# Kernel optimization log

Hardware: AMD Instinct MI355X
Metric: run time of the kernel (lower is better)

## Reference

```python
import jax, jax.numpy as jnp
import numpy as np

EMB = 512
H1, H2 = 300, 100


def setup_inputs() -> dict:
    key = jax.random.key(0)
    ks = jax.random.split(key, 12)
    B, N, M = 2, 256, 256
    inp = {
        "action_embedding": jax.random.normal(ks[0], (B, EMB, N), jnp.float32),
        "anchor_embedding": jax.random.normal(ks[1], (B, EMB, M), jnp.float32),
        "action_points": jax.random.normal(ks[2], (B, 3, N), jnp.float32),
        "anchor_points": jax.random.normal(ks[3], (B, 3, M), jnp.float32),
        # MLPKernel params: Linear(1024,300), Linear(300,100), Linear(100,1), stored as [in,out]
        "W1": jax.random.normal(ks[4], (2 * EMB, H1), jnp.float32) / np.sqrt(2 * EMB),
        "b1": jax.random.normal(ks[5], (H1,), jnp.float32) * 0.01,
        "W2": jax.random.normal(ks[6], (H1, H2), jnp.float32) / np.sqrt(H1),
        "b2": jax.random.normal(ks[7], (H2,), jnp.float32) * 0.01,
        "W3": jax.random.normal(ks[8], (H2, 1), jnp.float32) / np.sqrt(H2),
        "b3": jax.random.normal(ks[9], (1,), jnp.float32) * 0.01,
    }
    return inp


def _pairwise_radii(Phi_A, Phi_B, W1, b1, W2, b2, W3, b3):
    # MLPKernel: softplus((mlp(cat(a,b)) + mlp(cat(b,a))) / 2) over all (n, m) pairs.
    # Split first linear: cat(x1,x2) @ W1 == x1 @ Wa + x2 @ Wb  (no [B,N,M,1024] materialization).
    F = Phi_A.shape[-1]
    Wa, Wb = W1[:F], W1[F:]
    hA_a = jnp.einsum('bnf,fh->bnh', Phi_A, Wa)
    hA_b = jnp.einsum('bnf,fh->bnh', Phi_A, Wb)
    hB_a = jnp.einsum('bmf,fh->bmh', Phi_B, Wa)
    hB_b = jnp.einsum('bmf,fh->bmh', Phi_B, Wb)

    def mlp_rest(h):  # h: [B,N,M,H1] pre-bias first-layer activations
        h = jax.nn.relu(h + b1)
        h = jax.nn.relu(jnp.einsum('bnmh,hk->bnmk', h, W2) + b2)
        return jnp.einsum('bnmk,ko->bnmo', h, W3) + b3

    v1 = mlp_rest(hA_a[:, :, None, :] + hB_b[:, None, :, :])  # mlp(cat(A_n, B_m))
    v2 = mlp_rest(hB_a[:, None, :, :] + hA_b[:, :, None, :])  # mlp(cat(B_m, A_n))
    return jax.nn.softplus((v1 + v2) * 0.5)[..., 0]  # [B,N,M]


def _multilaterate(P, R, W):
    # Vectorized estimate_p over batch b and query point n.
    # P: [B,M,3] anchor points, R: [B,N,M] estimated radii, W: [B,M] weights.
    M = P.shape[1]
    norm2 = jnp.sum(P * P, axis=-1)                      # [B,M]  (Pt @ P)
    d = norm2[:, None, :] - R ** 2                       # [B,N,M]  PtP - r^2
    a = jnp.einsum('bm,bnm,bmd->bnd', W, d, P) / M       # [B,N,3]
    WPPt = jnp.einsum('bm,bmd,bme->bde', W, P, P) / M    # [B,3,3]  mean(W * P Pt)
    mWd = jnp.einsum('bm,bnm->bn', W, d) / M             # [B,N]    mean(W * (PtP - r^2))
    c = jnp.einsum('bm,bmd->bd', W, P) / M               # [B,3]
    # B @ c with B = -2*mean(W*PPt) - mean(W*d)*I
    Bc = -2.0 * jnp.einsum('bde,be->bd', WPPt, c)[:, None, :] - mWd[..., None] * c[:, None, :]
    cc = jnp.sum(c * c, axis=-1)                         # [B]
    f = a + Bc + 2.0 * cc[:, None, None] * c[:, None, :]  # [B,N,3]
    PPt_mean = jnp.einsum('bmd,bme->bde', P, P) / M       # unweighted mean(PPt)
    H = -2.0 * PPt_mean + 2.0 * jnp.einsum('bd,be->bde', c, c)  # [B,3,3]
    Hinv = jnp.linalg.inv(H)
    q = -jnp.einsum('bde,bne->bnd', Hinv, f)
    return q + c[:, None, :]                              # [B,N,3]


def reference(action_embedding, anchor_embedding, action_points, anchor_points,
              W1, b1, W2, b2, W3, b3):
    P_A = jnp.transpose(action_points, (0, 2, 1))    # [B,N,3]
    P_B = jnp.transpose(anchor_points, (0, 2, 1))    # [B,M,3]
    Phi_A = jnp.transpose(action_embedding, (0, 2, 1))  # [B,N,F]
    Phi_B = jnp.transpose(anchor_embedding, (0, 2, 1))  # [B,M,F]
    B_weights = jnp.ones(Phi_B.shape[:2], dtype=Phi_B.dtype)
    R_est = _pairwise_radii(Phi_A, Phi_B, W1, b1, W2, b2, W3, b3)
    P_A_B_pred = _multilaterate(P_B, R_est, B_weights)  # [B,N,3]
    flow = jnp.transpose(P_A_B_pred - P_A, (0, 2, 1))   # [B,3,N] == full_flow (pred_weight=False)
    return flow
```

## Files before the change

### kernel.cpp

```cpp
#include <hip/hip_runtime.h>
#include <hip/hip_bf16.h>
#include <math.h>

#define EMB 512
#define H1 300
#define H2 100
#define NB 2
#define NN 256
#define MM 256

#define OFF_HAA 0
#define OFF_HAB 153600
#define OFF_HBA 307200
#define OFF_HBB 460800
#define OFF_CST 616448
#define OFF_W2C 616512
#define OFF_B2P 634432
#define OFF_W3P 634544
#define OFF_ET  634656
#define OFF_W1T 896800
#define OFF_V   1060640

typedef __attribute__((ext_vector_type(8))) short bf16x8;
typedef __attribute__((ext_vector_type(4))) float f32x4;

static __device__ inline unsigned f2bfbits(float f) {
    union { float f; unsigned u; } v; v.f = f;
    return (v.u + 0x7fffu + ((v.u >> 16) & 1u)) >> 16;
}
static __device__ inline unsigned pack_bf2(float a, float b) {
    union { __hip_bfloat162 h; unsigned u; } cv;
    cv.h = __float22bfloat162_rn(make_float2(a, b));
    return cv.u;
}

__global__ __launch_bounds__(256) void k_setup(
    const float* __restrict__ W1, const float* __restrict__ W2,
    const float* __restrict__ b2, const float* __restrict__ W3,
    const float* __restrict__ actE, const float* __restrict__ ancE,
    const float* __restrict__ ancP, float* __restrict__ ws)
{
    __shared__ float Tf[32 * 36];
    __shared__ float red[4][13];
    int blk = blockIdx.x;
    int tid = threadIdx.x;

    if (blk < 320) {
        unsigned short* W1t = (unsigned short*)(ws + OFF_W1T);
        int h0 = (blk % 20) * 32, f0 = (blk / 20) * 32;
        int fr = tid >> 3, hc4 = (tid & 7) * 4;
        int hg = h0 + hc4;
        float4 v = make_float4(0.f, 0.f, 0.f, 0.f);
        if (hg < 600) {
            int half = (hg >= 300) ? 1 : 0;
            int hh = hg - half * 300;
            v = *(const float4*)&W1[(size_t)(half * EMB + f0 + fr) * H1 + hh];
        }
        *(float4*)&Tf[fr * 36 + hc4] = v;
        __syncthreads();
        int hr = tid >> 3, f4 = (tid & 7) * 4;
        float v0 = Tf[(f4 + 0) * 36 + hr];
        float v1 = Tf[(f4 + 1) * 36 + hr];
        float v2 = Tf[(f4 + 2) * 36 + hr];
        float v3 = Tf[(f4 + 3) * 36 + hr];
        uint2 pk = make_uint2(pack_bf2(v0, v1), pack_bf2(v2, v3));
        *(uint2*)&W1t[(size_t)(h0 + hr) * EMB + f0 + f4] = pk;
    } else if (blk < 832) {
        int i = blk - 320;
        unsigned short* Et = (unsigned short*)(ws + OFF_ET);
        int f0 = (i & 15) * 32;
        int n0 = ((i >> 4) & 7) * 32;
        int bs = i >> 7, b = bs >> 1, src = bs & 1;
        const float* E = (src == 0 ? actE : ancE) + (size_t)b * EMB * NN;
        int r = tid >> 3, c4 = (tid & 7) * 4;
        float4 v = *(const float4*)&E[(size_t)(f0 + r) * NN + n0 + c4];
        *(float4*)&Tf[r * 36 + c4] = v;
        __syncthreads();
        int nr = tid >> 3, f4 = (tid & 7) * 4;
        float v0 = Tf[(f4 + 0) * 36 + nr];
        float v1 = Tf[(f4 + 1) * 36 + nr];
        float v2 = Tf[(f4 + 2) * 36 + nr];
        float v3 = Tf[(f4 + 3) * 36 + nr];
        uint2 pk = make_uint2(pack_bf2(v0, v1), pack_bf2(v2, v3));
        *(uint2*)&Et[((size_t)(bs * NN) + n0 + nr) * EMB + f0 + f4] = pk;
    } else if (blk < 848) {
        int i = blk - 832;
        unsigned short* W2c = (unsigned short*)(ws + OFF_W2C);
        int start = i * 256 + tid;
        for (int idx = start; idx < 10*112*32; idx += 16 * 256) {
            int c  = idx / 3584;
            int r  = idx - c * 3584;
            int j  = r >> 5;
            int kk = r & 31;
            int k  = c * 32 + kk;
            float v = (j < H2 && k < H1) ? W2[k * H2 + j] : 0.0f;
            W2c[idx] = (unsigned short)f2bfbits(v);
        }
        if (i == 0 && tid < 112) {
            int j = tid;
            ws[OFF_B2P + j] = (j < H2) ? b2[j] : 0.0f;
            ws[OFF_W3P + j] = (j < H2) ? W3[j] : 0.0f;
        }
    } else {
        int b = blk - 848;
        float* cst = ws + OFF_CST;
        int m = tid;
        float px = ancP[b*3*MM + 0*MM + m];
        float py = ancP[b*3*MM + 1*MM + m];
        float pz = ancP[b*3*MM + 2*MM + m];
        float n2 = px*px + py*py + pz*pz;

        float v[13];
        v[0]=px; v[1]=py; v[2]=pz;
        v[3]=px*px; v[4]=px*py; v[5]=px*pz; v[6]=py*py; v[7]=py*pz; v[8]=pz*pz;
        v[9]=n2*px; v[10]=n2*py; v[11]=n2*pz; v[12]=n2;

        #pragma unroll
        for (int off = 32; off >= 1; off >>= 1) {
            #pragma unroll
            for (int q = 0; q < 13; q++) v[q] += __shfl_xor(v[q], off, 64);
        }
        int wave = tid >> 6, lane = tid & 63;
        if (lane == 0) {
            #pragma unroll
            for (int q = 0; q < 13; q++) red[wave][q] = v[q];
        }
        __syncthreads();
        if (tid == 0) {
            float s[13];
            #pragma unroll
            for (int q = 0; q < 13; q++)
                s[q] = red[0][q] + red[1][q] + red[2][q] + red[3][q];
            const float invM = 1.0f / MM;
            float c0 = s[0]*invM, c1 = s[1]*invM, c2 = s[2]*invM;
            float Pxx = s[3]*invM, Pxy = s[4]*invM, Pxz = s[5]*invM;
            float Pyy = s[6]*invM, Pyz = s[7]*invM, Pzz = s[8]*invM;

            float H00 = -2.0f*Pxx + 2.0f*c0*c0;
            float H01 = -2.0f*Pxy + 2.0f*c0*c1;
            float H02 = -2.0f*Pxz + 2.0f*c0*c2;
            float H11 = -2.0f*Pyy + 2.0f*c1*c1;
            float H12 = -2.0f*Pyz + 2.0f*c1*c2;
            float H22 = -2.0f*Pzz + 2.0f*c2*c2;
            float H10 = H01, H20 = H02, H21 = H12;

            float det = H00*(H11*H22 - H12*H21)
                      - H01*(H10*H22 - H12*H20)
                      + H02*(H10*H21 - H11*H20);
            float id = 1.0f / det;
            float i00 = (H11*H22 - H12*H21)*id;
            float i01 = (H02*H21 - H01*H22)*id;
            float i02 = (H01*H12 - H02*H11)*id;
            float i10 = (H12*H20 - H10*H22)*id;
            float i11 = (H00*H22 - H02*H20)*id;
            float i12 = (H02*H10 - H00*H12)*id;
            float i20 = (H10*H21 - H11*H20)*id;
            float i21 = (H01*H20 - H00*H21)*id;
            float i22 = (H00*H11 - H01*H10)*id;

            float t0x = -2.0f*(Pxx*c0 + Pxy*c1 + Pxz*c2);
            float t0y = -2.0f*(Pxy*c0 + Pyy*c1 + Pyz*c2);
            float t0z = -2.0f*(Pxz*c0 + Pyz*c1 + Pzz*c2);
            float cc = c0*c0 + c1*c1 + c2*c2;

            float* C = cst + b*32;
            C[0]=c0; C[1]=c1; C[2]=c2;
            C[3]=i00; C[4]=i01; C[5]=i02;
            C[6]=i10; C[7]=i11; C[8]=i12;
            C[9]=i20; C[10]=i21; C[11]=i22;
            C[12]=t0x; C[13]=t0y; C[14]=t0z;
            C[15]=cc;
            C[16]=s[9]*invM; C[17]=s[10]*invM; C[18]=s[11]*invM; C[19]=s[12]*invM;
        }
    }
}

__global__ __launch_bounds__(256) void k_hidden(
    float* __restrict__ ws, const float* __restrict__ b1)
{
    int bs = blockIdx.z, b = bs >> 1, src = bs & 1;
    int n0 = blockIdx.x * 16;
    int h0 = blockIdx.y * 64;
    const unsigned short* Et  = (const unsigned short*)(ws + OFF_ET)
                                + (size_t)(bs * NN) * EMB;
    const unsigned short* W1t = (const unsigned short*)(ws + OFF_W1T);
    float* outA = ws + (src == 0 ? OFF_HAA : OFF_HBA) + (size_t)b * NN * H1;
    float* outB = ws + (src == 0 ? OFF_HAB : OFF_HBB) + (size_t)b * NN * H1;

    __shared__ unsigned short EtL[16 * 40];
    __shared__ unsigned short W1tL[64 * 40];

    int tid = threadIdx.x;
    int lane = tid & 63, w = tid >> 6;
    int colj = lane & 15, quad = lane >> 4;

    int er  = tid >> 4, ek2 = (tid & 15) * 2;
    int wr  = tid >> 2, wk8 = (tid & 3) * 8;

    f32x4 acc = (f32x4){0.f, 0.f, 0.f, 0.f};

    for (int c = 0; c < 16; c++) {
        int k0 = c * 32;
        unsigned ev = *(const unsigned*)&Et[(size_t)(n0 + er) * EMB + k0 + ek2];
        uint4 wv = *(const uint4*)&W1t[(size_t)(h0 + wr) * EMB + k0 + wk8];
        __syncthreads();
        *(unsigned*)&EtL[er * 40 + ek2] = ev;
        *(uint4*)&W1tL[wr * 40 + wk8] = wv;
        __syncthreads();
        bf16x8 af = *(const bf16x8*)&EtL[colj * 40 + quad * 8];
        bf16x8 bf = *(const bf16x8*)&W1tL[(w * 16 + colj) * 40 + quad * 8];
        acc = __builtin_amdgcn_mfma_f32_16x16x32_bf16(af, bf, acc, 0, 0, 0);
    }

    int hg = h0 + w * 16 + colj;
    if (hg < 600) {
        int hh = (hg < 300) ? hg : hg - 300;
        float* o = (hg < 300) ? outA : outB;
        float bias = (src == 0) ? b1[hh] : 0.0f;
        #pragma unroll
        for (int r = 0; r < 4; r++) {
            int n = n0 + quad * 4 + r;
            o[(size_t)n * H1 + hh] = acc[r] + bias;
        }
    }
}

#define SH 308

__global__ __launch_bounds__(256, 2) void k_pair(
    const float* __restrict__ ws_f, const float* __restrict__ b3p,
    float* __restrict__ V)
{
    int bz = blockIdx.z, b = bz >> 1, p = bz & 1;
    int n0 = blockIdx.y * 16, m0 = blockIdx.x * 16;
    int tid = threadIdx.x;
    int lane = tid & 63, w = tid >> 6;
    int colj = lane & 15, quad = lane >> 4;

    __shared__ float hAf[16 * SH];
    __shared__ float hBf[16 * SH];

    const unsigned short* W2c = (const unsigned short*)(ws_f + OFF_W2C);
    float b2v[7], w3v[7];
    #pragma unroll
    for (int jt = 0; jt < 7; jt++) {
        b2v[jt] = ws_f[OFF_B2P + jt * 16 + colj];
        w3v[jt] = ws_f[OFF_W3P + jt * 16 + colj];
    }
    float b3val = b3p[0];

    const float* srcX = ws_f + (p == 0 ? OFF_HAA : OFF_HAB) + (size_t)(b*NN + n0) * H1;
    const float* srcY = ws_f + (p == 0 ? OFF_HBB : OFF_HBA) + (size_t)(b*NN + m0) * H1;

    for (int idx = tid; idx < 2464; idx += 256) {
        int a = (idx >= 1232) ? 1 : 0;
        int k = idx - a * 1232;
        int row, c4;
        float4 v = make_float4(0.f, 0.f, 0.f, 0.f);
        if (k < 1200) {
            row = k / 75; c4 = k - row * 75;
            v = *(const float4*)&(a ? srcY : srcX)[row * H1 + c4 * 4];
        } else {
            int j = k - 1200;
            row = j >> 1; c4 = 75 + (j & 1);
        }
        float* dst = (a ? hBf : hAf) + row * SH + c4 * 4;
        *(float4*)dst = v;
    }
    __syncthreads();

    f32x4 acc[4][7];
    #pragma unroll
    for (int i = 0; i < 4; i++)
        #pragma unroll
        for (int jt = 0; jt < 7; jt++)
            acc[i][jt] = (f32x4){0.f,0.f,0.f,0.f};

    #pragma unroll
    for (int c = 0; c < 10; c++) {
        bf16x8 bfr[7];
        #pragma unroll
        for (int jt = 0; jt < 7; jt++)
            bfr[jt] = *(const bf16x8*)&W2c[c * 3584 + (jt * 16 + colj) * 32 + quad * 8];

        float4 hb0 = *(const float4*)&hBf[colj * SH + c * 32 + quad * 8];
        float4 hb1 = *(const float4*)&hBf[colj * SH + c * 32 + quad * 8 + 4];

        #pragma unroll
        for (int i = 0; i < 4; i++) {
            const float* xa = &hAf[(w * 4 + i) * SH + c * 32 + quad * 8];
            float4 ha0 = *(const float4*)&xa[0];
            float4 ha1 = *(const float4*)&xa[4];
            union { unsigned u[4]; bf16x8 v; } af;
            af.u[0] = pack_bf2(fmaxf(ha0.x + hb0.x, 0.f), fmaxf(ha0.y + hb0.y, 0.f));
            af.u[1] = pack_bf2(fmaxf(ha0.z + hb0.z, 0.f), fmaxf(ha0.w + hb0.w, 0.f));
            af.u[2] = pack_bf2(fmaxf(ha1.x + hb1.x, 0.f), fmaxf(ha1.y + hb1.y, 0.f));
            af.u[3] = pack_bf2(fmaxf(ha1.z + hb1.z, 0.f), fmaxf(ha1.w + hb1.w, 0.f));
            #pragma unroll
            for (int jt = 0; jt < 7; jt++)
                acc[i][jt] = __builtin_amdgcn_mfma_f32_16x16x32_bf16(
                    af.v, bfr[jt], acc[i][jt], 0, 0, 0);
        }
    }

    float vsum[4][4];
    #pragma unroll
    for (int i = 0; i < 4; i++)
        #pragma unroll
        for (int r = 0; r < 4; r++) vsum[i][r] = 0.0f;
    #pragma unroll
    for (int i = 0; i < 4; i++)
        #pragma unroll
        for (int jt = 0; jt < 7; jt++)
            #pragma unroll
            for (int r = 0; r < 4; r++)
                vsum[i][r] = fmaf(fmaxf(acc[i][jt][r] + b2v[jt], 0.f),
                                  w3v[jt], vsum[i][r]);

    #pragma unroll
    for (int i = 0; i < 4; i++)
        #pragma unroll
        for (int r = 0; r < 4; r++) {
            float v = vsum[i][r];
            v += __shfl_xor(v, 1, 16);
            v += __shfl_xor(v, 2, 16);
            v += __shfl_xor(v, 4, 16);
            v += __shfl_xor(v, 8, 16);
            vsum[i][r] = v;
        }

    if (colj == 0) {
        #pragma unroll
        for (int i = 0; i < 4; i++) {
            int n = n0 + w * 4 + i;
            float4 o;
            o.x = 0.5f * (vsum[i][0] + b3val);
            o.y = 0.5f * (vsum[i][1] + b3val);
            o.z = 0.5f * (vsum[i][2] + b3val);
            o.w = 0.5f * (vsum[i][3] + b3val);
            *(float4*)&V[(((size_t)p * NB + b) * NN + n) * MM + m0 + quad * 4] = o;
        }
    }
}

__global__ void k_finish(const float* __restrict__ V, const float* __restrict__ ancP,
                         const float* __restrict__ cst, const float* __restrict__ actP,
                         float* __restrict__ out)
{
    int b = blockIdx.y;
    int n = blockIdx.x * 16 + (threadIdx.x >> 4);
    int ml = threadIdx.x & 15;
    const float* v0 = V + (((size_t)0 * NB + b) * NN + n) * MM;
    const float* v1 = V + (((size_t)1 * NB + b) * NN + n) * MM;
    float s0 = 0.f, s1 = 0.f, s2 = 0.f, s3 = 0.f;
    #pragma unroll
    for (int k = 0; k < 16; k++) {
        int m = ml + k * 16;
        float x = v0[m] + v1[m];
        float R = fmaxf(x, 0.f) + log1pf(expf(-fabsf(x)));
        float r2 = R * R;
        float px = ancP[b*3*MM + 0*MM + m];
        float py = ancP[b*3*MM + 1*MM + m];
        float pz = ancP[b*3*MM + 2*MM + m];
        s0 = fmaf(r2, px, s0);
        s1 = fmaf(r2, py, s1);
        s2 = fmaf(r2, pz, s2);
        s3 += r2;
    }
    #pragma unroll
    for (int off = 8; off >= 1; off >>= 1) {
        s0 += __shfl_xor(s0, off, 16);
        s1 += __shfl_xor(s1, off, 16);
        s2 += __shfl_xor(s2, off, 16);
        s3 += __shfl_xor(s3, off, 16);
    }
    if (ml == 0) {
        const float* C = cst + b*32;
        float c0=C[0], c1=C[1], c2=C[2];
        float t0x=C[12], t0y=C[13], t0z=C[14];
        float cc=C[15];
        float SnP0=C[16], SnP1=C[17], SnP2=C[18], Sn=C[19];

        const float invM = 1.0f / MM;
        float a0 = SnP0 - s0*invM;
        float a1 = SnP1 - s1*invM;
        float a2 = SnP2 - s2*invM;
        float mWd = Sn - s3*invM;

        float f0 = a0 + t0x - mWd*c0 + 2.0f*cc*c0;
        float f1 = a1 + t0y - mWd*c1 + 2.0f*cc*c1;
        float f2 = a2 + t0z - mWd*c2 + 2.0f*cc*c2;

        float q0 = -(C[3]*f0 + C[4]*f1 + C[5]*f2);
        float q1 = -(C[6]*f0 + C[7]*f1 + C[8]*f2);
        float q2 = -(C[9]*f0 + C[10]*f1 + C[11]*f2);

        float p0 = q0 + c0, p1 = q1 + c1, p2 = q2 + c2;

        out[b*3*NN + 0*NN + n] = p0 - actP[b*3*NN + 0*NN + n];
        out[b*3*NN + 1*NN + n] = p1 - actP[b*3*NN + 1*NN + n];
        out[b*3*NN + 2*NN + n] = p2 - actP[b*3*NN + 2*NN + n];
    }
}

extern "C" void kernel_launch(void* const* d_in, const int* in_sizes, int n_in,
                              void* d_out, int out_size, void* d_ws, size_t ws_size,
                              hipStream_t stream)
{
    const float* actE = (const float*)d_in[0];
    const float* ancE = (const float*)d_in[1];
    const float* actP = (const float*)d_in[2];
    const float* ancP = (const float*)d_in[3];
    const float* W1   = (const float*)d_in[4];
    const float* b1   = (const float*)d_in[5];
    const float* W2   = (const float*)d_in[6];
    const float* b2   = (const float*)d_in[7];
    const float* W3   = (const float*)d_in[8];
    const float* b3   = (const float*)d_in[9];
    float* ws  = (float*)d_ws;
    float* out = (float*)d_out;

    k_setup <<<850, 256, 0, stream>>>(W1, W2, b2, W3, actE, ancE, ancP, ws);
    k_hidden<<<dim3(16, 10, 4), 256, 0, stream>>>(ws, b1);
    k_pair  <<<dim3(16, 16, NB*2), 256, 0, stream>>>(ws, b3, ws + OFF_V);
    k_finish<<<dim3(16, NB), 256, 0, stream>>>(ws + OFF_V, ancP, ws + OFF_CST, actP, out);
}
```

Before: 125.5 us.

## Fuse softplus-multilateration finish into pair kernel via atomics and last-block reduction

The pair kernel now runs both MLP orderings (p=0,1) inside one block and accumulates vsum across them. It then applies softplus and reduces r² moments per query point with atomicAdd into a small workspace buffer. A global counter picks the last block, which computes the final multilateration output, so the V intermediate buffer and the separate finish kernel are gone. This removes a launch and the V write/read traffic. In exchange the grid halves, each block does twice the serial work, and atomics plus a serial tail block are added.

```diff
diff --git a/kernel.cpp b/kernel.cpp
--- a/kernel.cpp
+++ b/kernel.cpp
@@ -13,13 +13,14 @@
 #define OFF_HAB 153600
 #define OFF_HBA 307200
 #define OFF_HBB 460800
+#define OFF_S   614400
 #define OFF_CST 616448
 #define OFF_W2C 616512
 #define OFF_B2P 634432
 #define OFF_W3P 634544
 #define OFF_ET  634656
 #define OFF_W1T 896800
-#define OFF_V   1060640
+#define OFF_CNT 1060640
 
 typedef __attribute__((ext_vector_type(8))) short bf16x8;
 typedef __attribute__((ext_vector_type(4))) float f32x4;
@@ -96,10 +97,16 @@
             float v = (j < H2 && k < H1) ? W2[k * H2 + j] : 0.0f;
             W2c[idx] = (unsigned short)f2bfbits(v);
         }
-        if (i == 0 && tid < 112) {
-            int j = tid;
-            ws[OFF_B2P + j] = (j < H2) ? b2[j] : 0.0f;
-            ws[OFF_W3P + j] = (j < H2) ? W3[j] : 0.0f;
+        if (i == 0) {
+            if (tid < 112) {
+                int j = tid;
+                ws[OFF_B2P + j] = (j < H2) ? b2[j] : 0.0f;
+                ws[OFF_W3P + j] = (j < H2) ? W3[j] : 0.0f;
+            }
+            #pragma unroll
+            for (int q = 0; q < 8; q++)
+                ws[OFF_S + q * 256 + tid] = 0.0f;
+            if (tid == 0) *(unsigned*)(ws + OFF_CNT) = 0u;
         }
     } else {
         int b = blk - 848;
@@ -228,10 +235,11 @@
 #define SH 308
 
 __global__ __launch_bounds__(256, 2) void k_pair(
-    const float* __restrict__ ws_f, const float* __restrict__ b3p,
-    float* __restrict__ V)
+    float* __restrict__ ws_f, const float* __restrict__ b3p,
+    const float* __restrict__ ancP, const float* __restrict__ actP,
+    float* __restrict__ out)
 {
-    int bz = blockIdx.z, b = bz >> 1, p = bz & 1;
+    int b  = blockIdx.z;
     int n0 = blockIdx.y * 16, m0 = blockIdx.x * 16;
     int tid = threadIdx.x;
     int lane = tid & 63, w = tid >> 6;
@@ -239,6 +247,7 @@
 
     __shared__ float hAf[16 * SH];
     __shared__ float hBf[16 * SH];
+    __shared__ int lastflag;
 
     const unsigned short* W2c = (const unsigned short*)(ws_f + OFF_W2C);
     float b2v[7], w3v[7];
@@ -248,59 +257,13 @@
         w3v[jt] = ws_f[OFF_W3P + jt * 16 + colj];
     }
     float b3val = b3p[0];
-
-    const float* srcX = ws_f + (p == 0 ? OFF_HAA : OFF_HAB) + (size_t)(b*NN + n0) * H1;
-    const float* srcY = ws_f + (p == 0 ? OFF_HBB : OFF_HBA) + (size_t)(b*NN + m0) * H1;
-
-    for (int idx = tid; idx < 2464; idx += 256) {
-        int a = (idx >= 1232) ? 1 : 0;
-        int k = idx - a * 1232;
-        int row, c4;
-        float4 v = make_float4(0.f, 0.f, 0.f, 0.f);
-        if (k < 1200) {
-            row = k / 75; c4 = k - row * 75;
-            v = *(const float4*)&(a ? srcY : srcX)[row * H1 + c4 * 4];
-        } else {
-            int j = k - 1200;
-            row = j >> 1; c4 = 75 + (j & 1);
-        }
-        float* dst = (a ? hBf : hAf) + row * SH + c4 * 4;
-        *(float4*)dst = v;
-    }
-    __syncthreads();
-
-    f32x4 acc[4][7];
+    float pxv[4], pyv[4], pzv[4];
     #pragma unroll
-    for (int i = 0; i < 4; i++)
-        #pragma unroll
-        for (int jt = 0; jt < 7; jt++)
-            acc[i][jt] = (f32x4){0.f,0.f,0.f,0.f};
-
-    #pragma unroll
-    for (int c = 0; c < 10; c++) {
-        bf16x8 bfr[7];
-        #pragma unroll
-        for (int jt = 0; jt < 7; jt++)
-            bfr[jt] = *(const bf16x8*)&W2c[c * 3584 + (jt * 16 + colj) * 32 + quad * 8];
-
-        float4 hb0 = *(const float4*)&hBf[colj * SH + c * 32 + quad * 8];
-        float4 hb1 = *(const float4*)&hBf[colj * SH + c * 32 + quad * 8 + 4];
-
-        #pragma unroll
-        for (int i = 0; i < 4; i++) {
-            const float* xa = &hAf[(w * 4 + i) * SH + c * 32 + quad * 8];
-            float4 ha0 = *(const float4*)&xa[0];
-            float4 ha1 = *(const float4*)&xa[4];
-            union { unsigned u[4]; bf16x8 v; } af;
-            af.u[0] = pack_bf2(fmaxf(ha0.x + hb0.x, 0.f), fmaxf(ha0.y + hb0.y, 0.f));
-            af.u[1] = pack_bf2(fmaxf(ha0.z + hb0.z, 0.f), fmaxf(ha0.w + hb0.w, 0.f));
-            af.u[2] = pack_bf2(fmaxf(ha1.x + hb1.x, 0.f), fmaxf(ha1.y + hb1.y, 0.f));
-            af.u[3] = pack_bf2(fmaxf(ha1.z + hb1.z, 0.f), fmaxf(ha1.w + hb1.w, 0.f));
-            #pragma unroll
-            for (int jt = 0; jt < 7; jt++)
-                acc[i][jt] = __builtin_amdgcn_mfma_f32_16x16x32_bf16(
-                    af.v, bfr[jt], acc[i][jt], 0, 0, 0);
-        }
+    for (int r = 0; r < 4; r++) {
+        int m = m0 + quad * 4 + r;
+        pxv[r] = ancP[b*3*MM + 0*MM + m];
+        pyv[r] = ancP[b*3*MM + 1*MM + m];
+        pzv[r] = ancP[b*3*MM + 2*MM + m];
     }
 
     float vsum[4][4];
@@ -308,14 +271,73 @@
     for (int i = 0; i < 4; i++)
         #pragma unroll
         for (int r = 0; r < 4; r++) vsum[i][r] = 0.0f;
-    #pragma unroll
-    for (int i = 0; i < 4; i++)
-        #pragma unroll
-        for (int jt = 0; jt < 7; jt++)
-            #pragma unroll
-            for (int r = 0; r < 4; r++)
-                vsum[i][r] = fmaf(fmaxf(acc[i][jt][r] + b2v[jt], 0.f),
-                                  w3v[jt], vsum[i][r]);
+
+    #pragma unroll 1
+    for (int p = 0; p < 2; p++) {
+        const float* srcX = ws_f + (p == 0 ? OFF_HAA : OFF_HAB) + (size_t)(b*NN + n0) * H1;
+        const float* srcY = ws_f + (p == 0 ? OFF_HBB : OFF_HBA) + (size_t)(b*NN + m0) * H1;
+
+        __syncthreads();
+        for (int idx = tid; idx < 2464; idx += 256) {
+            int a = (idx >= 1232) ? 1 : 0;
+            int k = idx - a * 1232;
+            int row, c4;
+            float4 v = make_float4(0.f, 0.f, 0.f, 0.f);
+            if (k < 1200) {
+                row = k / 75; c4 = k - row * 75;
+                v = *(const float4*)&(a ? srcY : srcX)[row * H1 + c4 * 4];
+            } else {
+                int j = k - 1200;
+                row = j >> 1; c4 = 75 + (j & 1);
+            }
+            float* dst = (a ? hBf : hAf) + row * SH + c4 * 4;
+            *(float4*)dst = v;
+        }
+        __syncthreads();
+
+        f32x4 acc[4][7];
+        #pragma unroll
+        for (int i = 0; i < 4; i++)
+            #pragma unroll
+            for (int jt = 0; jt < 7; jt++)
+                acc[i][jt] = (f32x4){0.f,0.f,0.f,0.f};
+
+        #pragma unroll
+        for (int c = 0; c < 10; c++) {
+            bf16x8 bfr[7];
+            #pragma unroll
+            for (int jt = 0; jt < 7; jt++)
+                bfr[jt] = *(const bf16x8*)&W2c[c * 3584 + (jt * 16 + colj) * 32 + quad * 8];
+
+            float4 hb0 = *(const float4*)&hBf[colj * SH + c * 32 + quad * 8];
+            float4 hb1 = *(const float4*)&hBf[colj * SH + c * 32 + quad * 8 + 4];
+
+            #pragma unroll
+            for (int i = 0; i < 4; i++) {
+                const float* xa = &hAf[(w * 4 + i) * SH + c * 32 + quad * 8];
+                float4 ha0 = *(const float4*)&xa[0];
+                float4 ha1 = *(const float4*)&xa[4];
+                union { unsigned u[4]; bf16x8 v; } af;
+                af.u[0] = pack_bf2(fmaxf(ha0.x + hb0.x, 0.f), fmaxf(ha0.y + hb0.y, 0.f));
+                af.u[1] = pack_bf2(fmaxf(ha0.z + hb0.z, 0.f), fmaxf(ha0.w + hb0.w, 0.f));
+                af.u[2] = pack_bf2(fmaxf(ha1.x + hb1.x, 0.f), fmaxf(ha1.y + hb1.y, 0.f));
+                af.u[3] = pack_bf2(fmaxf(ha1.z + hb1.z, 0.f), fmaxf(ha1.w + hb1.w, 0.f));
+                #pragma unroll
+                for (int jt = 0; jt < 7; jt++)
+                    acc[i][jt] = __builtin_amdgcn_mfma_f32_16x16x32_bf16(
+                        af.v, bfr[jt], acc[i][jt], 0, 0, 0);
+            }
+        }
+
+        #pragma unroll
+        for (int i = 0; i < 4; i++)
+            #pragma unroll
+            for (int jt = 0; jt < 7; jt++)
+                #pragma unroll
+                for (int r = 0; r < 4; r++)
+                    vsum[i][r] = fmaf(fmaxf(acc[i][jt][r] + b2v[jt], 0.f),
+                                      w3v[jt], vsum[i][r]);
+    }
 
     #pragma unroll
     for (int i = 0; i < 4; i++)
@@ -329,53 +351,53 @@
             vsum[i][r] = v;
         }
 
-    if (colj == 0) {
-        #pragma unroll
-        for (int i = 0; i < 4; i++) {
+    float* S = ws_f + OFF_S;
+    #pragma unroll
+    for (int i = 0; i < 4; i++) {
+        float s0 = 0.f, s1 = 0.f, s2 = 0.f, s3 = 0.f;
+        #pragma unroll
+        for (int r = 0; r < 4; r++) {
+            float x = 0.5f * vsum[i][r] + b3val;
+            float R = fmaxf(x, 0.f) + log1pf(expf(-fabsf(x)));
+            float r2 = R * R;
+            s0 = fmaf(r2, pxv[r], s0);
+            s1 = fmaf(r2, pyv[r], s1);
+            s2 = fmaf(r2, pzv[r], s2);
+            s3 += r2;
+        }
+        s0 += __shfl_xor(s0, 16, 64); s0 += __shfl_xor(s0, 32, 64);
+        s1 += __shfl_xor(s1, 16, 64); s1 += __shfl_xor(s1, 32, 64);
+        s2 += __shfl_xor(s2, 16, 64); s2 += __shfl_xor(s2, 32, 64);
+        s3 += __shfl_xor(s3, 16, 64); s3 += __shfl_xor(s3, 32, 64);
+        if (lane == 0) {
             int n = n0 + w * 4 + i;
-            float4 o;
-            o.x = 0.5f * (vsum[i][0] + b3val);
-            o.y = 0.5f * (vsum[i][1] + b3val);
-            o.z = 0.5f * (vsum[i][2] + b3val);
-            o.w = 0.5f * (vsum[i][3] + b3val);
-            *(float4*)&V[(((size_t)p * NB + b) * NN + n) * MM + m0 + quad * 4] = o;
-        }
-    }
-}
-
-__global__ void k_finish(const float* __restrict__ V, const float* __restrict__ ancP,
-                         const float* __restrict__ cst, const float* __restrict__ actP,
-                         float* __restrict__ out)
-{
-    int b = blockIdx.y;
-    int n = blockIdx.x * 16 + (threadIdx.x >> 4);
-    int ml = threadIdx.x & 15;
-    const float* v0 = V + (((size_t)0 * NB + b) * NN + n) * MM;
-    const float* v1 = V + (((size_t)1 * NB + b) * NN + n) * MM;
-    float s0 = 0.f, s1 = 0.f, s2 = 0.f, s3 = 0.f;
-    #pragma unroll
-    for (int k = 0; k < 16; k++) {
-        int m = ml + k * 16;
-        float x = v0[m] + v1[m];
-        float R = fmaxf(x, 0.f) + log1pf(expf(-fabsf(x)));
-        float r2 = R * R;
-        float px = ancP[b*3*MM + 0*MM + m];
-        float py = ancP[b*3*MM + 1*MM + m];
-        float pz = ancP[b*3*MM + 2*MM + m];
-        s0 = fmaf(r2, px, s0);
-        s1 = fmaf(r2, py, s1);
-        s2 = fmaf(r2, pz, s2);
-        s3 += r2;
-    }
-    #pragma unroll
-    for (int off = 8; off >= 1; off >>= 1) {
-        s0 += __shfl_xor(s0, off, 16);
-        s1 += __shfl_xor(s1, off, 16);
-        s2 += __shfl_xor(s2, off, 16);
-        s3 += __shfl_xor(s3, off, 16);
-    }
-    if (ml == 0) {
-        const float* C = cst + b*32;
+            float* sp = S + (size_t)(b*NN + n) * 4;
+            atomicAdd(sp + 0, s0);
+            atomicAdd(sp + 1, s1);
+            atomicAdd(sp + 2, s2);
+            atomicAdd(sp + 3, s3);
+        }
+    }
+
+    __threadfence();
+    if (tid == 0) {
+        unsigned old = atomicAdd((unsigned*)(ws_f + OFF_CNT), 1u);
+        lastflag = (old == 511u);
+    }
+    __syncthreads();
+    if (!lastflag) return;
+    __threadfence();
+
+    const float* cst = ws_f + OFF_CST;
+    for (int bb = 0; bb < NB; bb++) {
+        int n = tid;
+        float* sp = S + (size_t)(bb*NN + n) * 4;
+        float s0 = atomicAdd(sp + 0, 0.0f);
+        float s1 = atomicAdd(sp + 1, 0.0f);
+        float s2 = atomicAdd(sp + 2, 0.0f);
+        float s3 = atomicAdd(sp + 3, 0.0f);
+
+        const float* C = cst + bb*32;
         float c0=C[0], c1=C[1], c2=C[2];
         float t0x=C[12], t0y=C[13], t0z=C[14];
         float cc=C[15];
@@ -397,9 +419,9 @@
 
         float p0 = q0 + c0, p1 = q1 + c1, p2 = q2 + c2;
 
-        out[b*3*NN + 0*NN + n] = p0 - actP[b*3*NN + 0*NN + n];
-        out[b*3*NN + 1*NN + n] = p1 - actP[b*3*NN + 1*NN + n];
-        out[b*3*NN + 2*NN + n] = p2 - actP[b*3*NN + 2*NN + n];
+        out[bb*3*NN + 0*NN + n] = p0 - actP[bb*3*NN + 0*NN + n];
+        out[bb*3*NN + 1*NN + n] = p1 - actP[bb*3*NN + 1*NN + n];
+        out[bb*3*NN + 2*NN + n] = p2 - actP[bb*3*NN + 2*NN + n];
     }
 }
 
@@ -422,6 +444,5 @@
 
     k_setup <<<850, 256, 0, stream>>>(W1, W2, b2, W3, actE, ancE, ancP, ws);
     k_hidden<<<dim3(16, 10, 4), 256, 0, stream>>>(ws, b1);
-    k_pair  <<<dim3(16, 16, NB*2), 256, 0, stream>>>(ws, b3, ws + OFF_V);
-    k_finish<<<dim3(16, NB), 256, 0, stream>>>(ws + OFF_V, ancP, ws + OFF_CST, actP, out);
-}
+    k_pair  <<<dim3(16, 16, NB), 256, 0, stream>>>(ws, b3, ancP, actP, out);
+}
```

Result: slower. 178.6 us (+42.3%).
